# Optimization experiments

Hardware: AMD Instinct MI355X
Metric: run time of the kernel (lower is better)

## Reference

```python
import jax, jax.numpy as jnp
import numpy as np
import math

NUM_HEADS = 16
ROPE_BASE = 10000.0


def _rotate_half(x):
    d = x.shape[-1] // 2
    return jnp.concatenate([-x[..., d:], x[..., :d]], axis=-1)


def setup_inputs() -> dict:
    key = jax.random.key(0)
    ks = jax.random.split(key, 6)
    B, S, H = 2, 2048, 2048
    x = jax.random.normal(ks[0], (B, S, H), dtype=jnp.float32)
    # xavier_uniform for square [H,H]: limit = sqrt(6/(H+H))
    lim = math.sqrt(6.0 / (H + H))
    Wq = jax.random.uniform(ks[1], (H, H), minval=-lim, maxval=lim, dtype=jnp.float32)
    Wk = jax.random.uniform(ks[2], (H, H), minval=-lim, maxval=lim, dtype=jnp.float32)
    Wv = jax.random.uniform(ks[3], (H, H), minval=-lim, maxval=lim, dtype=jnp.float32)
    Wo = jax.random.uniform(ks[4], (H, H), minval=-lim, maxval=lim, dtype=jnp.float32)
    # bias_matrix initialized as tril(randn*0.02), matching _init_weights
    bias_matrix = jnp.tril(jax.random.normal(ks[5], (S, S), dtype=jnp.float32) * 0.02)
    return {"x": x, "Wq": Wq, "Wk": Wk, "Wv": Wv, "Wo": Wo, "bias_matrix": bias_matrix}


def reference(x, Wq, Wk, Wv, Wo, bias_matrix):
    B, S, hidden = x.shape
    H = NUM_HEADS
    D = hidden // H

    # projections (torch Linear: y = x @ W.T)
    def proj(W):
        return jnp.einsum('bsh,eh->bse', x, W).reshape(B, S, H, D).transpose(0, 2, 1, 3)

    q, k, v = proj(Wq), proj(Wk), proj(Wv)  # [B,H,S,D]

    # rotary embeddings
    inv_freq = 1.0 / (ROPE_BASE ** (jnp.arange(0, D, 2, dtype=jnp.float32) / D))
    t = jnp.arange(S, dtype=jnp.float32)
    freqs = t[:, None] * inv_freq[None, :]          # [S, D/2]
    emb = jnp.concatenate([freqs, freqs], axis=-1)  # [S, D]
    cos = jnp.cos(emb)[None, None]                  # [1,1,S,D]
    sin = jnp.sin(emb)[None, None]

    q = q * cos + _rotate_half(q) * sin
    k = k * cos + _rotate_half(k) * sin

    # contextual bias: bias_matrix[:S,:S], broadcast over batch & heads
    bias = bias_matrix[:S, :S][None, None]          # [1,1,S,S]
    bmean = jnp.mean(bias, axis=-1, keepdims=True) * 0.1  # [1,1,S,1]
    q = q + bmean
    k = k + bmean

    scores = jnp.einsum('bhqd,bhkd->bhqk', q, k) / math.sqrt(D)
    scores = scores + bias

    causal = jnp.triu(jnp.ones((S, S), dtype=bool), k=1)
    scores = jnp.where(causal[None, None], -jnp.inf, scores)

    attn_weights = jax.nn.softmax(scores, axis=-1)  # [B,H,S,S]
    attn_out = jnp.einsum('bhqk,bhkd->bhqd', attn_weights, v)
    attn_out = attn_out.transpose(0, 2, 1, 3).reshape(B, S, hidden)
    output = jnp.einsum('bsh,eh->bse', attn_out, Wo)
    return output, attn_weights
```

## Files before the change

kernel.cpp:

```cpp
#include <hip/hip_runtime.h>
#include <hip/hip_bf16.h>

typedef __bf16 bf16_t;
typedef __bf16 bf16x8 __attribute__((ext_vector_type(8)));
typedef float f32x4 __attribute__((ext_vector_type(4)));

#define SEQ 2048
#define HID 2048
#define NH 16
#define DH 128
#define BATCH 2

typedef __attribute__((address_space(1))) const unsigned int g_u32;
typedef __attribute__((address_space(3))) unsigned int l_u32;
#define GLOAD_LDS16(g, l) __builtin_amdgcn_global_load_lds((g_u32*)(g), (l_u32*)(l), 16, 0, 0)

__device__ __forceinline__ unsigned short f2bf(float f) {
  return __builtin_bit_cast(unsigned short, (__bf16)f);
}

__global__ void k_cast_bf16(const float4* __restrict__ in, ushort4* __restrict__ out, int n4) {
  int i = blockIdx.x * 256 + threadIdx.x;
  if (i >= n4) return;
  float4 v = in[i];
  ushort4 o;
  o.x = f2bf(v.x); o.y = f2bf(v.y); o.z = f2bf(v.z); o.w = f2bf(v.w);
  out[i] = o;
}

__global__ void k_bmean(const float* __restrict__ bias, float* __restrict__ bm) {
  int s = blockIdx.x;
  int t = threadIdx.x;
  const float4* row = (const float4*)(bias + (size_t)s * SEQ);
  float acc = 0.f;
  for (int c = t; c < SEQ / 4; c += 256) { float4 v = row[c]; acc += (v.x + v.y) + (v.z + v.w); }
  for (int off = 1; off < 64; off <<= 1) acc += __shfl_xor(acc, off);
  __shared__ float red[4];
  if ((t & 63) == 0) red[t >> 6] = acc;
  __syncthreads();
  if (t == 0) bm[s] = (red[0] + red[1] + red[2] + red[3]) * (0.1f / SEQ);
}

template <int EPI>
__global__ __launch_bounds__(256, 2) void k_gemm_bt(const bf16_t* __restrict__ A,
                                                    const bf16_t* __restrict__ B,
                                                    void* __restrict__ C,
                                                    int M, int N, int K) {
  __shared__ ushort As[128 * 64];
  __shared__ ushort Bs[128 * 64];
  const int tid = threadIdx.x;
  const int lane = tid & 63, wave = tid >> 6;
  const int m16 = lane & 15, quad = lane >> 4;
  const int wm = (wave >> 1) * 64, wn = (wave & 1) * 64;
  const int bm0 = blockIdx.y * 128, bn0 = blockIdx.x * 128;

  f32x4 acc[4][4];
  for (int i = 0; i < 4; ++i)
    for (int j = 0; j < 4; ++j) acc[i][j] = (f32x4){0.f, 0.f, 0.f, 0.f};

  const int NT = K / 64;
  for (int kt = 0; kt < NT; ++kt) {
    __syncthreads();
    size_t k0 = (size_t)kt * 64;
    for (int it = 0; it < 4; ++it) {
      int g = it * 256 + tid;
      int r = g >> 3;
      int c8 = (g & 7) ^ (r & 7);
      int base = (it * 256 + wave * 64) * 8;
      GLOAD_LDS16(A + (size_t)(bm0 + r) * K + k0 + c8 * 8, &As[base]);
      GLOAD_LDS16(B + (size_t)(bn0 + r) * K + k0 + c8 * 8, &Bs[base]);
    }
    __syncthreads();
    for (int ks = 0; ks < 2; ++ks) {
      bf16x8 af[4], bfr[4];
      for (int i = 0; i < 4; ++i) {
        int row = wm + i * 16 + m16;
        af[i] = *(const bf16x8*)&As[row * 64 + (((ks * 4 + quad) ^ (row & 7)) * 8)];
      }
      for (int j = 0; j < 4; ++j) {
        int row = wn + j * 16 + m16;
        bfr[j] = *(const bf16x8*)&Bs[row * 64 + (((ks * 4 + quad) ^ (row & 7)) * 8)];
      }
      for (int i = 0; i < 4; ++i)
        for (int j = 0; j < 4; ++j)
          acc[i][j] = __builtin_amdgcn_mfma_f32_16x16x32_bf16(af[i], bfr[j], acc[i][j], 0, 0, 0);
    }
  }
  for (int i = 0; i < 4; ++i)
    for (int j = 0; j < 4; ++j)
      for (int r = 0; r < 4; ++r) {
        int row = bm0 + wm + i * 16 + quad * 4 + r;
        int col = bn0 + wn + j * 16 + m16;
        float v = acc[i][j][r];
        if (EPI == 0) ((float*)C)[(size_t)row * N + col] = v;
        else          ((bf16_t*)C)[(size_t)row * N + col] = (bf16_t)v;
      }
}

__global__ void k_vtrans(const bf16_t* __restrict__ Vr, bf16_t* __restrict__ Vt) {
  __shared__ ushort T[64 * 72];
  const int tid = threadIdx.x;
  const int s0 = blockIdx.x * 64, c0 = blockIdx.y * 64, b = blockIdx.z;
  const int h = c0 >> 7, d0 = c0 & (DH - 1);
  int r = tid >> 2, cc = (tid & 3) * 16;
  const bf16_t* src = Vr + ((size_t)(b * SEQ + s0 + r)) * HID + c0 + cc;
  *(uint4*)&T[r * 72 + cc] = *(const uint4*)src;
  *(uint4*)&T[r * 72 + cc + 8] = *(const uint4*)(src + 8);
  __syncthreads();
  int dr = tid >> 2, sc0 = (tid & 3) * 16;
  ushort tmp[16];
  for (int e = 0; e < 16; ++e) tmp[e] = T[(sc0 + e) * 72 + dr];
  bf16_t* dst = Vt + ((size_t)(b * NH + h) * DH + d0 + dr) * SEQ + s0 + sc0;
  *(uint4*)dst = *(uint4*)&tmp[0];
  *(uint4*)(dst + 8) = *(uint4*)&tmp[8];
}

__global__ void k_rope(const float* __restrict__ Qf, const float* __restrict__ Kf,
                       const float* __restrict__ bm,
                       bf16_t* __restrict__ Qb, bf16_t* __restrict__ Kb) {
  int idx = blockIdx.x * 256 + threadIdx.x;
  int row = idx >> 10, p = idx & 1023;
  int h = p >> 6, i = p & 63;
  int s = row & (SEQ - 1);
  float invf = powf(10000.f, -(float)i * (1.f / 64.f));
  float ang = (float)s * invf;
  float sn, cs;
  sincosf(ang, &sn, &cs);
  float b = bm[s];
  size_t o1 = (size_t)row * HID + h * DH + i;
  size_t o2 = o1 + 64;
  float q1 = Qf[o1], q2 = Qf[o2];
  Qb[o1] = (bf16_t)(q1 * cs - q2 * sn + b);
  Qb[o2] = (bf16_t)(q2 * cs + q1 * sn + b);
  float k1 = Kf[o1], k2 = Kf[o2];
  Kb[o1] = (bf16_t)(k1 * cs - k2 * sn + b);
  Kb[o2] = (bf16_t)(k2 * cs + k1 * sn + b);
}

__global__ __launch_bounds__(256, 3) void k_attn(const bf16_t* __restrict__ Qb,
                                                 const bf16_t* __restrict__ Kb,
                                                 const bf16_t* __restrict__ Vt,
                                                 const float* __restrict__ bias,
                                                 float* __restrict__ P,
                                                 bf16_t* __restrict__ AO) {
  __shared__ ushort Qs[64 * 128];
  __shared__ ushort Ks[64 * 128];
  __shared__ ushort Ps[64 * 72];
  __shared__ ushort Bs[64 * 68];

  const int tid = threadIdx.x;
  const int lane = tid & 63, wave = tid >> 6;
  const int m16 = lane & 15, quad = lane >> 4;
  const int qb = (int)gridDim.x - 1 - (int)blockIdx.x;
  const int h = blockIdx.y, b = blockIdx.z;
  const int q0 = qb * 64;
  const int wq = wave * 16;
  const float scale = 0.08838834764831845f;

  const bf16_t* Qg = Qb + ((size_t)(b * SEQ + q0)) * HID + (size_t)h * DH;
  for (int it = 0; it < 4; ++it) {
    int g = it * 256 + tid;
    int r = g >> 4;
    int c16 = (g & 15) ^ (r & 15);
    GLOAD_LDS16(Qg + (size_t)r * HID + c16 * 8, &Qs[(it * 256 + wave * 64) * 8]);
  }

  const bf16_t* Kbase = Kb + ((size_t)b * SEQ) * HID + (size_t)h * DH;
  const float* bg = bias + (size_t)q0 * SEQ;

  float m_ln[4], l_ln[4];
  for (int r = 0; r < 4; ++r) { m_ln[r] = -1e30f; l_ln[r] = 0.f; }

  const int bR = tid >> 4, bC = (tid & 15) * 4;
  float4 bpre[4];
  for (int it = 0; it < 4; ++it)
    bpre[it] = *(const float4*)(bg + (size_t)(bR + it * 16) * SEQ + bC);

  for (int kt = 0; kt <= qb; ++kt) {
    __syncthreads();
    const bf16_t* Kg = Kbase + (size_t)(kt * 64) * HID;
    for (int it = 0; it < 4; ++it) {
      int g = it * 256 + tid;
      int r = g >> 4;
      int c16 = (g & 15) ^ (r & 15);
      GLOAD_LDS16(Kg + (size_t)r * HID + c16 * 8, &Ks[(it * 256 + wave * 64) * 8]);
    }
    for (int it = 0; it < 4; ++it) {
      ushort4 o;
      o.x = f2bf(bpre[it].x); o.y = f2bf(bpre[it].y); o.z = f2bf(bpre[it].z); o.w = f2bf(bpre[it].w);
      *(ushort4*)&Bs[(bR + it * 16) * 68 + bC] = o;
    }
    __syncthreads();
    if (kt < qb)
      for (int it = 0; it < 4; ++it)
        bpre[it] = *(const float4*)(bg + (size_t)(bR + it * 16) * SEQ + (kt + 1) * 64 + bC);

    f32x4 sc[4];
    for (int j = 0; j < 4; ++j) sc[j] = (f32x4){0.f, 0.f, 0.f, 0.f};
    for (int ks = 0; ks < 4; ++ks) {
      int qrow = wq + m16;
      bf16x8 af = *(const bf16x8*)&Qs[qrow * 128 + (((ks * 4 + quad) ^ (qrow & 15)) * 8)];
      for (int j = 0; j < 4; ++j) {
        int krow = j * 16 + m16;
        bf16x8 bfr = *(const bf16x8*)&Ks[krow * 128 + (((ks * 4 + quad) ^ (krow & 15)) * 8)];
        sc[j] = __builtin_amdgcn_mfma_f32_16x16x32_bf16(af, bfr, sc[j], 0, 0, 0);
      }
    }
    for (int r = 0; r < 4; ++r) {
      int rl = wq + quad * 4 + r, qi = q0 + rl;
      float v[4], mx = m_ln[r];
      for (int j = 0; j < 4; ++j) {
        int ki = kt * 64 + j * 16 + m16;
        float bv = (float)(*(const bf16_t*)&Bs[rl * 68 + j * 16 + m16]);
        float xv = sc[j][r] * scale + bv;
        v[j] = (ki > qi) ? -1e30f : xv;
        mx = fmaxf(mx, v[j]);
      }
      float corr = __expf(m_ln[r] - mx);
      float s = __expf(v[0] - mx) + __expf(v[1] - mx) + __expf(v[2] - mx) + __expf(v[3] - mx);
      l_ln[r] = l_ln[r] * corr + s;
      m_ln[r] = mx;
    }
  }
  float mrow[4], linv[4];
  for (int r = 0; r < 4; ++r) {
    float m = m_ln[r], l = l_ln[r];
    for (int off = 1; off < 16; off <<= 1) {
      float mo = __shfl_xor(m, off), lo = __shfl_xor(l, off);
      float mn = fmaxf(m, mo);
      l = l * __expf(m - mn) + lo * __expf(mo - mn);
      m = mn;
    }
    mrow[r] = m; linv[r] = 1.f / l;
  }

  f32x4 oacc[8];
  for (int d = 0; d < 8; ++d) oacc[d] = (f32x4){0.f, 0.f, 0.f, 0.f};
  float* Pg = P + (((size_t)(b * NH + h)) * SEQ + q0) * SEQ;
  const bf16_t* Vbase = Vt + ((size_t)(b * NH + h)) * DH * SEQ;

  for (int it = 0; it < 4; ++it)
    bpre[it] = *(const float4*)(bg + (size_t)(bR + it * 16) * SEQ + bC);

  for (int kt = 0; kt <= qb; ++kt) {
    __syncthreads();
    const bf16_t* Kg = Kbase + (size_t)(kt * 64) * HID;
    for (int it = 0; it < 4; ++it) {
      int g = it * 256 + tid;
      int r = g >> 4;
      int c16 = (g & 15) ^ (r & 15);
      GLOAD_LDS16(Kg + (size_t)r * HID + c16 * 8, &Ks[(it * 256 + wave * 64) * 8]);
    }
    for (int it = 0; it < 4; ++it) {
      ushort4 o;
      o.x = f2bf(bpre[it].x); o.y = f2bf(bpre[it].y); o.z = f2bf(bpre[it].z); o.w = f2bf(bpre[it].w);
      *(ushort4*)&Bs[(bR + it * 16) * 68 + bC] = o;
    }
    __syncthreads();
    if (kt < qb)
      for (int it = 0; it < 4; ++it)
        bpre[it] = *(const float4*)(bg + (size_t)(bR + it * 16) * SEQ + (kt + 1) * 64 + bC);

    f32x4 sc[4];
    for (int j = 0; j < 4; ++j) sc[j] = (f32x4){0.f, 0.f, 0.f, 0.f};
    for (int ks = 0; ks < 4; ++ks) {
      int qrow = wq + m16;
      bf16x8 af = *(const bf16x8*)&Qs[qrow * 128 + (((ks * 4 + quad) ^ (qrow & 15)) * 8)];
      for (int j = 0; j < 4; ++j) {
        int krow = j * 16 + m16;
        bf16x8 bfr = *(const bf16x8*)&Ks[krow * 128 + (((ks * 4 + quad) ^ (krow & 15)) * 8)];
        sc[j] = __builtin_amdgcn_mfma_f32_16x16x32_bf16(af, bfr, sc[j], 0, 0, 0);
      }
    }

    bf16x8 vf0[8];
    for (int dt = 0; dt < 8; ++dt)
      vf0[dt] = *(const bf16x8*)(Vbase + (size_t)(dt * 16 + m16) * SEQ + kt * 64 + quad * 8);

    for (int r = 0; r < 4; ++r) {
      int rl = wq + quad * 4 + r, qi = q0 + rl;
      for (int j = 0; j < 4; ++j) {
        int ki = kt * 64 + j * 16 + m16;
        float bv = (float)(*(const bf16_t*)&Bs[rl * 68 + j * 16 + m16]);
        float xv = sc[j][r] * scale + bv;
        float p = (ki > qi) ? 0.f : __expf(xv - mrow[r]) * linv[r];
        Pg[(size_t)rl * SEQ + ki] = p;
        Ps[rl * 72 + j * 16 + m16] = f2bf(p);
      }
    }

    bf16x8 vf1[8];
    for (int dt = 0; dt < 8; ++dt)
      vf1[dt] = *(const bf16x8*)(Vbase + (size_t)(dt * 16 + m16) * SEQ + kt * 64 + 32 + quad * 8);

    {
      bf16x8 pf = *(const bf16x8*)&Ps[(wq + m16) * 72 + quad * 8];
      for (int dt = 0; dt < 8; ++dt)
        oacc[dt] = __builtin_amdgcn_mfma_f32_16x16x32_bf16(pf, vf0[dt], oacc[dt], 0, 0, 0);
      pf = *(const bf16x8*)&Ps[(wq + m16) * 72 + 32 + quad * 8];
      for (int dt = 0; dt < 8; ++dt)
        oacc[dt] = __builtin_amdgcn_mfma_f32_16x16x32_bf16(pf, vf1[dt], oacc[dt], 0, 0, 0);
    }
  }

  bf16_t* AOg = AO + ((size_t)(b * SEQ + q0)) * HID + (size_t)h * DH;
  for (int r = 0; r < 4; ++r) {
    int rl = wq + quad * 4 + r;
    for (int dt = 0; dt < 8; ++dt)
      AOg[(size_t)rl * HID + dt * 16 + m16] = (bf16_t)oacc[dt][r];
  }

  int kz0 = (qb + 1) * 64;
  for (int r = 0; r < 64; ++r) {
    float4* dst = (float4*)(Pg + (size_t)r * SEQ);
    for (int c = kz0 / 4 + tid; c < SEQ / 4; c += 256) dst[c] = make_float4(0.f, 0.f, 0.f, 0.f);
  }
}

extern "C" void kernel_launch(void* const* d_in, const int* in_sizes, int n_in,
                              void* d_out, int out_size, void* d_ws, size_t ws_size,
                              hipStream_t stream) {
  const float* x = (const float*)d_in[0];
  const float* Wq = (const float*)d_in[1];
  const float* Wk = (const float*)d_in[2];
  const float* Wv = (const float*)d_in[3];
  const float* Wo = (const float*)d_in[4];
  const float* bias = (const float*)d_in[5];

  float* out = (float*)d_out;
  float* P = out + (size_t)BATCH * SEQ * HID;
  float* Qf = P;
  float* Kf = P + (size_t)BATCH * SEQ * HID;
  bf16_t* Vr = (bf16_t*)(P + 2 * (size_t)BATCH * SEQ * HID);

  char* w = (char*)d_ws;
  bf16_t* xb = (bf16_t*)w;  w += (size_t)BATCH * SEQ * HID * 2;
  bf16_t* Wqb = (bf16_t*)w; w += (size_t)HID * HID * 2;
  bf16_t* Wkb = (bf16_t*)w; w += (size_t)HID * HID * 2;
  bf16_t* Wvb = (bf16_t*)w; w += (size_t)HID * HID * 2;
  bf16_t* Wob = (bf16_t*)w; w += (size_t)HID * HID * 2;
  bf16_t* Qb = (bf16_t*)w;  w += (size_t)BATCH * SEQ * HID * 2;
  bf16_t* Kb = (bf16_t*)w;  w += (size_t)BATCH * SEQ * HID * 2;
  bf16_t* Vt = (bf16_t*)w;  w += (size_t)BATCH * SEQ * HID * 2;
  bf16_t* AO = (bf16_t*)w;  w += (size_t)BATCH * SEQ * HID * 2;
  float* bm = (float*)w;    w += (size_t)SEQ * 4;

  const int n4x = BATCH * SEQ * HID / 4;
  const int n4w = HID * HID / 4;
  k_cast_bf16<<<(n4x + 255) / 256, 256, 0, stream>>>((const float4*)x, (ushort4*)xb, n4x);
  k_cast_bf16<<<(n4w + 255) / 256, 256, 0, stream>>>((const float4*)Wq, (ushort4*)Wqb, n4w);
  k_cast_bf16<<<(n4w + 255) / 256, 256, 0, stream>>>((const float4*)Wk, (ushort4*)Wkb, n4w);
  k_cast_bf16<<<(n4w + 255) / 256, 256, 0, stream>>>((const float4*)Wv, (ushort4*)Wvb, n4w);
  k_cast_bf16<<<(n4w + 255) / 256, 256, 0, stream>>>((const float4*)Wo, (ushort4*)Wob, n4w);
  k_bmean<<<SEQ, 256, 0, stream>>>(bias, bm);

  dim3 gg(HID / 128, BATCH * SEQ / 128);
  k_gemm_bt<0><<<gg, 256, 0, stream>>>(xb, Wqb, Qf, BATCH * SEQ, HID, HID);
  k_gemm_bt<0><<<gg, 256, 0, stream>>>(xb, Wkb, Kf, BATCH * SEQ, HID, HID);
  k_gemm_bt<1><<<gg, 256, 0, stream>>>(xb, Wvb, Vr, BATCH * SEQ, HID, HID);

  k_vtrans<<<dim3(SEQ / 64, HID / 64, BATCH), 256, 0, stream>>>(Vr, Vt);
  k_rope<<<(BATCH * SEQ * HID / 2) / 256, 256, 0, stream>>>(Qf, Kf, bm, Qb, Kb);

  k_attn<<<dim3(SEQ / 64, NH, BATCH), 256, 0, stream>>>(Qb, Kb, Vt, bias, P, AO);

  k_gemm_bt<0><<<gg, 256, 0, stream>>>(AO, Wob, out, BATCH * SEQ, HID, HID);
}
```

Baseline: 1.231 ms.

## Load Q, K and bias directly into registers, drop LDS staging and barriers

Removes the shared-memory staging of Q, K and the bias tile, along with the two __syncthreads per key tile. Each wave now loads its Q fragments once into registers and reads K fragments and bias values straight from global memory per tile. The probability matrix stores and the zero-fill of the masked region now use nontemporal stores, and many loops gain unroll pragmas. This cuts LDS traffic and synchronisation, at the cost of redundant K loads across the four waves (now served by cache) and less coalesced bias reads in float instead of bf16.

```diff
diff --git a/kernel.cpp b/kernel.cpp
--- a/kernel.cpp
+++ b/kernel.cpp
@@ -143,10 +143,7 @@
                                                  const float* __restrict__ bias,
                                                  float* __restrict__ P,
                                                  bf16_t* __restrict__ AO) {
-  __shared__ ushort Qs[64 * 128];
-  __shared__ ushort Ks[64 * 128];
   __shared__ ushort Ps[64 * 72];
-  __shared__ ushort Bs[64 * 68];
 
   const int tid = threadIdx.x;
   const int lane = tid & 63, wave = tid >> 6;
@@ -157,62 +154,49 @@
   const int wq = wave * 16;
   const float scale = 0.08838834764831845f;
 
-  const bf16_t* Qg = Qb + ((size_t)(b * SEQ + q0)) * HID + (size_t)h * DH;
-  for (int it = 0; it < 4; ++it) {
-    int g = it * 256 + tid;
-    int r = g >> 4;
-    int c16 = (g & 15) ^ (r & 15);
-    GLOAD_LDS16(Qg + (size_t)r * HID + c16 * 8, &Qs[(it * 256 + wave * 64) * 8]);
-  }
-
-  const bf16_t* Kbase = Kb + ((size_t)b * SEQ) * HID + (size_t)h * DH;
-  const float* bg = bias + (size_t)q0 * SEQ;
+  const bf16_t* Qg = Qb + ((size_t)(b * SEQ + q0 + wq + m16)) * HID + (size_t)h * DH;
+  bf16x8 qf[4];
+#pragma unroll
+  for (int ks = 0; ks < 4; ++ks) qf[ks] = *(const bf16x8*)(Qg + ks * 32 + quad * 8);
+
+  const bf16_t* Kbase = Kb + ((size_t)b * SEQ) * HID + (size_t)h * DH + quad * 8;
+  const float* bl = bias + (size_t)(q0 + wq + quad * 4) * SEQ + m16;
 
   float m_ln[4], l_ln[4];
+#pragma unroll
   for (int r = 0; r < 4; ++r) { m_ln[r] = -1e30f; l_ln[r] = 0.f; }
 
-  const int bR = tid >> 4, bC = (tid & 15) * 4;
-  float4 bpre[4];
-  for (int it = 0; it < 4; ++it)
-    bpre[it] = *(const float4*)(bg + (size_t)(bR + it * 16) * SEQ + bC);
-
   for (int kt = 0; kt <= qb; ++kt) {
-    __syncthreads();
-    const bf16_t* Kg = Kbase + (size_t)(kt * 64) * HID;
-    for (int it = 0; it < 4; ++it) {
-      int g = it * 256 + tid;
-      int r = g >> 4;
-      int c16 = (g & 15) ^ (r & 15);
-      GLOAD_LDS16(Kg + (size_t)r * HID + c16 * 8, &Ks[(it * 256 + wave * 64) * 8]);
-    }
-    for (int it = 0; it < 4; ++it) {
-      ushort4 o;
-      o.x = f2bf(bpre[it].x); o.y = f2bf(bpre[it].y); o.z = f2bf(bpre[it].z); o.w = f2bf(bpre[it].w);
-      *(ushort4*)&Bs[(bR + it * 16) * 68 + bC] = o;
-    }
-    __syncthreads();
-    if (kt < qb)
-      for (int it = 0; it < 4; ++it)
-        bpre[it] = *(const float4*)(bg + (size_t)(bR + it * 16) * SEQ + (kt + 1) * 64 + bC);
+    const bf16_t* Kg = Kbase + (size_t)(kt * 64 + m16) * HID;
+    float bv[4][4];
+#pragma unroll
+    for (int r = 0; r < 4; ++r)
+#pragma unroll
+      for (int j = 0; j < 4; ++j) bv[r][j] = bl[(size_t)r * SEQ + kt * 64 + j * 16];
 
     f32x4 sc[4];
+#pragma unroll
     for (int j = 0; j < 4; ++j) sc[j] = (f32x4){0.f, 0.f, 0.f, 0.f};
-    for (int ks = 0; ks < 4; ++ks) {
-      int qrow = wq + m16;
-      bf16x8 af = *(const bf16x8*)&Qs[qrow * 128 + (((ks * 4 + quad) ^ (qrow & 15)) * 8)];
-      for (int j = 0; j < 4; ++j) {
-        int krow = j * 16 + m16;
-        bf16x8 bfr = *(const bf16x8*)&Ks[krow * 128 + (((ks * 4 + quad) ^ (krow & 15)) * 8)];
-        sc[j] = __builtin_amdgcn_mfma_f32_16x16x32_bf16(af, bfr, sc[j], 0, 0, 0);
-      }
-    }
+#pragma unroll
+    for (int j = 0; j < 4; ++j) {
+      const bf16_t* kr = Kg + (size_t)(j * 16) * HID;
+      bf16x8 k0 = *(const bf16x8*)(kr);
+      bf16x8 k1 = *(const bf16x8*)(kr + 32);
+      bf16x8 k2 = *(const bf16x8*)(kr + 64);
+      bf16x8 k3 = *(const bf16x8*)(kr + 96);
+      sc[j] = __builtin_amdgcn_mfma_f32_16x16x32_bf16(qf[0], k0, sc[j], 0, 0, 0);
+      sc[j] = __builtin_amdgcn_mfma_f32_16x16x32_bf16(qf[1], k1, sc[j], 0, 0, 0);
+      sc[j] = __builtin_amdgcn_mfma_f32_16x16x32_bf16(qf[2], k2, sc[j], 0, 0, 0);
+      sc[j] = __builtin_amdgcn_mfma_f32_16x16x32_bf16(qf[3], k3, sc[j], 0, 0, 0);
+    }
+#pragma unroll
     for (int r = 0; r < 4; ++r) {
-      int rl = wq + quad * 4 + r, qi = q0 + rl;
+      int qi = q0 + wq + quad * 4 + r;
       float v[4], mx = m_ln[r];
+#pragma unroll
       for (int j = 0; j < 4; ++j) {
         int ki = kt * 64 + j * 16 + m16;
-        float bv = (float)(*(const bf16_t*)&Bs[rl * 68 + j * 16 + m16]);
-        float xv = sc[j][r] * scale + bv;
+        float xv = sc[j][r] * scale + bv[r][j];
         v[j] = (ki > qi) ? -1e30f : xv;
         mx = fmaxf(mx, v[j]);
       }
@@ -223,6 +207,7 @@
     }
   }
   float mrow[4], linv[4];
+#pragma unroll
   for (int r = 0; r < 4; ++r) {
     float m = m_ln[r], l = l_ln[r];
     for (int off = 1; off < 16; off <<= 1) {
@@ -235,85 +220,85 @@
   }
 
   f32x4 oacc[8];
+#pragma unroll
   for (int d = 0; d < 8; ++d) oacc[d] = (f32x4){0.f, 0.f, 0.f, 0.f};
   float* Pg = P + (((size_t)(b * NH + h)) * SEQ + q0) * SEQ;
   const bf16_t* Vbase = Vt + ((size_t)(b * NH + h)) * DH * SEQ;
 
-  for (int it = 0; it < 4; ++it)
-    bpre[it] = *(const float4*)(bg + (size_t)(bR + it * 16) * SEQ + bC);
-
   for (int kt = 0; kt <= qb; ++kt) {
-    __syncthreads();
-    const bf16_t* Kg = Kbase + (size_t)(kt * 64) * HID;
-    for (int it = 0; it < 4; ++it) {
-      int g = it * 256 + tid;
-      int r = g >> 4;
-      int c16 = (g & 15) ^ (r & 15);
-      GLOAD_LDS16(Kg + (size_t)r * HID + c16 * 8, &Ks[(it * 256 + wave * 64) * 8]);
-    }
-    for (int it = 0; it < 4; ++it) {
-      ushort4 o;
-      o.x = f2bf(bpre[it].x); o.y = f2bf(bpre[it].y); o.z = f2bf(bpre[it].z); o.w = f2bf(bpre[it].w);
-      *(ushort4*)&Bs[(bR + it * 16) * 68 + bC] = o;
-    }
-    __syncthreads();
-    if (kt < qb)
-      for (int it = 0; it < 4; ++it)
-        bpre[it] = *(const float4*)(bg + (size_t)(bR + it * 16) * SEQ + (kt + 1) * 64 + bC);
+    const bf16_t* Kg = Kbase + (size_t)(kt * 64 + m16) * HID;
+    float bv[4][4];
+#pragma unroll
+    for (int r = 0; r < 4; ++r)
+#pragma unroll
+      for (int j = 0; j < 4; ++j) bv[r][j] = bl[(size_t)r * SEQ + kt * 64 + j * 16];
 
     f32x4 sc[4];
+#pragma unroll
     for (int j = 0; j < 4; ++j) sc[j] = (f32x4){0.f, 0.f, 0.f, 0.f};
-    for (int ks = 0; ks < 4; ++ks) {
-      int qrow = wq + m16;
-      bf16x8 af = *(const bf16x8*)&Qs[qrow * 128 + (((ks * 4 + quad) ^ (qrow & 15)) * 8)];
-      for (int j = 0; j < 4; ++j) {
-        int krow = j * 16 + m16;
-        bf16x8 bfr = *(const bf16x8*)&Ks[krow * 128 + (((ks * 4 + quad) ^ (krow & 15)) * 8)];
-        sc[j] = __builtin_amdgcn_mfma_f32_16x16x32_bf16(af, bfr, sc[j], 0, 0, 0);
-      }
+#pragma unroll
+    for (int j = 0; j < 4; ++j) {
+      const bf16_t* kr = Kg + (size_t)(j * 16) * HID;
+      bf16x8 k0 = *(const bf16x8*)(kr);
+      bf16x8 k1 = *(const bf16x8*)(kr + 32);
+      bf16x8 k2 = *(const bf16x8*)(kr + 64);
+      bf16x8 k3 = *(const bf16x8*)(kr + 96);
+      sc[j] = __builtin_amdgcn_mfma_f32_16x16x32_bf16(qf[0], k0, sc[j], 0, 0, 0);
+      sc[j] = __builtin_amdgcn_mfma_f32_16x16x32_bf16(qf[1], k1, sc[j], 0, 0, 0);
+      sc[j] = __builtin_amdgcn_mfma_f32_16x16x32_bf16(qf[2], k2, sc[j], 0, 0, 0);
+      sc[j] = __builtin_amdgcn_mfma_f32_16x16x32_bf16(qf[3], k3, sc[j], 0, 0, 0);
     }
 
     bf16x8 vf0[8];
+#pragma unroll
     for (int dt = 0; dt < 8; ++dt)
       vf0[dt] = *(const bf16x8*)(Vbase + (size_t)(dt * 16 + m16) * SEQ + kt * 64 + quad * 8);
 
+#pragma unroll
     for (int r = 0; r < 4; ++r) {
       int rl = wq + quad * 4 + r, qi = q0 + rl;
+#pragma unroll
       for (int j = 0; j < 4; ++j) {
         int ki = kt * 64 + j * 16 + m16;
-        float bv = (float)(*(const bf16_t*)&Bs[rl * 68 + j * 16 + m16]);
-        float xv = sc[j][r] * scale + bv;
+        float xv = sc[j][r] * scale + bv[r][j];
         float p = (ki > qi) ? 0.f : __expf(xv - mrow[r]) * linv[r];
-        Pg[(size_t)rl * SEQ + ki] = p;
+        __builtin_nontemporal_store(p, Pg + (size_t)rl * SEQ + ki);
         Ps[rl * 72 + j * 16 + m16] = f2bf(p);
       }
     }
 
     bf16x8 vf1[8];
+#pragma unroll
     for (int dt = 0; dt < 8; ++dt)
       vf1[dt] = *(const bf16x8*)(Vbase + (size_t)(dt * 16 + m16) * SEQ + kt * 64 + 32 + quad * 8);
 
     {
       bf16x8 pf = *(const bf16x8*)&Ps[(wq + m16) * 72 + quad * 8];
+#pragma unroll
       for (int dt = 0; dt < 8; ++dt)
         oacc[dt] = __builtin_amdgcn_mfma_f32_16x16x32_bf16(pf, vf0[dt], oacc[dt], 0, 0, 0);
       pf = *(const bf16x8*)&Ps[(wq + m16) * 72 + 32 + quad * 8];
+#pragma unroll
       for (int dt = 0; dt < 8; ++dt)
         oacc[dt] = __builtin_amdgcn_mfma_f32_16x16x32_bf16(pf, vf1[dt], oacc[dt], 0, 0, 0);
     }
   }
 
   bf16_t* AOg = AO + ((size_t)(b * SEQ + q0)) * HID + (size_t)h * DH;
+#pragma unroll
   for (int r = 0; r < 4; ++r) {
     int rl = wq + quad * 4 + r;
+#pragma unroll
     for (int dt = 0; dt < 8; ++dt)
       AOg[(size_t)rl * HID + dt * 16 + m16] = (bf16_t)oacc[dt][r];
   }
 
   int kz0 = (qb + 1) * 64;
+  f32x4 z4 = (f32x4){0.f, 0.f, 0.f, 0.f};
   for (int r = 0; r < 64; ++r) {
-    float4* dst = (float4*)(Pg + (size_t)r * SEQ);
-    for (int c = kz0 / 4 + tid; c < SEQ / 4; c += 256) dst[c] = make_float4(0.f, 0.f, 0.f, 0.f);
+    f32x4* dst = (f32x4*)(Pg + (size_t)r * SEQ);
+    for (int c = kz0 / 4 + tid; c < SEQ / 4; c += 256)
+      __builtin_nontemporal_store(z4, dst + c);
   }
 }
 
```

Result: slower. 1.451 ms (+17.9%).

## Double-buffer K and bias tiles, precast bias to bf16, pair causal query tiles

Applied to the files above, without the earlier changes.

The bias matrix is now cast to bf16 once, into the reused x workspace, and staged into LDS with direct global-to-LDS loads. K and bias tiles are double-buffered so the next tile's loads overlap the current tile's MFMA work. Each block now handles two query tiles (qt and 31-qt) to balance causal work, using a grid half the size. The costs are more LDS per block and launch_bounds lowered to 2 blocks per CU, which may reduce occupancy, plus one extra cast kernel.

```diff
diff --git a/kernel.cpp b/kernel.cpp
--- a/kernel.cpp
+++ b/kernel.cpp
@@ -137,183 +137,201 @@
   Kb[o2] = (bf16_t)(k2 * cs + k1 * sn + b);
 }
 
-__global__ __launch_bounds__(256, 3) void k_attn(const bf16_t* __restrict__ Qb,
+__global__ __launch_bounds__(256, 2) void k_attn(const bf16_t* __restrict__ Qb,
                                                  const bf16_t* __restrict__ Kb,
                                                  const bf16_t* __restrict__ Vt,
-                                                 const float* __restrict__ bias,
+                                                 const bf16_t* __restrict__ Bb,
                                                  float* __restrict__ P,
                                                  bf16_t* __restrict__ AO) {
   __shared__ ushort Qs[64 * 128];
-  __shared__ ushort Ks[64 * 128];
+  __shared__ ushort Ks[2][64 * 128];
+  __shared__ ushort Bs[2][64 * 64];
   __shared__ ushort Ps[64 * 72];
-  __shared__ ushort Bs[64 * 68];
 
   const int tid = threadIdx.x;
   const int lane = tid & 63, wave = tid >> 6;
   const int m16 = lane & 15, quad = lane >> 4;
-  const int qb = (int)gridDim.x - 1 - (int)blockIdx.x;
   const int h = blockIdx.y, b = blockIdx.z;
-  const int q0 = qb * 64;
   const int wq = wave * 16;
   const float scale = 0.08838834764831845f;
 
-  const bf16_t* Qg = Qb + ((size_t)(b * SEQ + q0)) * HID + (size_t)h * DH;
-  for (int it = 0; it < 4; ++it) {
-    int g = it * 256 + tid;
-    int r = g >> 4;
-    int c16 = (g & 15) ^ (r & 15);
-    GLOAD_LDS16(Qg + (size_t)r * HID + c16 * 8, &Qs[(it * 256 + wave * 64) * 8]);
-  }
-
   const bf16_t* Kbase = Kb + ((size_t)b * SEQ) * HID + (size_t)h * DH;
-  const float* bg = bias + (size_t)q0 * SEQ;
-
-  float m_ln[4], l_ln[4];
-  for (int r = 0; r < 4; ++r) { m_ln[r] = -1e30f; l_ln[r] = 0.f; }
-
-  const int bR = tid >> 4, bC = (tid & 15) * 4;
-  float4 bpre[4];
-  for (int it = 0; it < 4; ++it)
-    bpre[it] = *(const float4*)(bg + (size_t)(bR + it * 16) * SEQ + bC);
-
-  for (int kt = 0; kt <= qb; ++kt) {
-    __syncthreads();
+  const bf16_t* Vbase = Vt + ((size_t)(b * NH + h)) * DH * SEQ;
+
+  auto stageK = [&](int kt, int buf) {
     const bf16_t* Kg = Kbase + (size_t)(kt * 64) * HID;
+#pragma unroll
     for (int it = 0; it < 4; ++it) {
       int g = it * 256 + tid;
       int r = g >> 4;
       int c16 = (g & 15) ^ (r & 15);
-      GLOAD_LDS16(Kg + (size_t)r * HID + c16 * 8, &Ks[(it * 256 + wave * 64) * 8]);
-    }
-    for (int it = 0; it < 4; ++it) {
-      ushort4 o;
-      o.x = f2bf(bpre[it].x); o.y = f2bf(bpre[it].y); o.z = f2bf(bpre[it].z); o.w = f2bf(bpre[it].w);
-      *(ushort4*)&Bs[(bR + it * 16) * 68 + bC] = o;
-    }
+      GLOAD_LDS16(Kg + (size_t)r * HID + c16 * 8, &Ks[buf][(it * 256 + wave * 64) * 8]);
+    }
+  };
+
+  for (int half = 0; half < 2; ++half) {
+    const int qt = half ? (int)blockIdx.x : 31 - (int)blockIdx.x;
+    const int q0 = qt * 64;
+    const bf16_t* Bgq = Bb + (size_t)q0 * SEQ;
+
+    auto stageB = [&](int kt, int buf) {
+      const bf16_t* Bg = Bgq + kt * 64;
+#pragma unroll
+      for (int it = 0; it < 2; ++it) {
+        int g = it * 256 + tid;
+        int r = g >> 3;
+        int c8 = (g & 7) ^ (r & 7);
+        GLOAD_LDS16(Bg + (size_t)r * SEQ + c8 * 8, &Bs[buf][(it * 256 + wave * 64) * 8]);
+      }
+    };
+
     __syncthreads();
-    if (kt < qb)
-      for (int it = 0; it < 4; ++it)
-        bpre[it] = *(const float4*)(bg + (size_t)(bR + it * 16) * SEQ + (kt + 1) * 64 + bC);
-
-    f32x4 sc[4];
-    for (int j = 0; j < 4; ++j) sc[j] = (f32x4){0.f, 0.f, 0.f, 0.f};
-    for (int ks = 0; ks < 4; ++ks) {
-      int qrow = wq + m16;
-      bf16x8 af = *(const bf16x8*)&Qs[qrow * 128 + (((ks * 4 + quad) ^ (qrow & 15)) * 8)];
-      for (int j = 0; j < 4; ++j) {
-        int krow = j * 16 + m16;
-        bf16x8 bfr = *(const bf16x8*)&Ks[krow * 128 + (((ks * 4 + quad) ^ (krow & 15)) * 8)];
-        sc[j] = __builtin_amdgcn_mfma_f32_16x16x32_bf16(af, bfr, sc[j], 0, 0, 0);
-      }
-    }
-    for (int r = 0; r < 4; ++r) {
-      int rl = wq + quad * 4 + r, qi = q0 + rl;
-      float v[4], mx = m_ln[r];
-      for (int j = 0; j < 4; ++j) {
-        int ki = kt * 64 + j * 16 + m16;
-        float bv = (float)(*(const bf16_t*)&Bs[rl * 68 + j * 16 + m16]);
-        float xv = sc[j][r] * scale + bv;
-        v[j] = (ki > qi) ? -1e30f : xv;
-        mx = fmaxf(mx, v[j]);
-      }
-      float corr = __expf(m_ln[r] - mx);
-      float s = __expf(v[0] - mx) + __expf(v[1] - mx) + __expf(v[2] - mx) + __expf(v[3] - mx);
-      l_ln[r] = l_ln[r] * corr + s;
-      m_ln[r] = mx;
-    }
-  }
-  float mrow[4], linv[4];
-  for (int r = 0; r < 4; ++r) {
-    float m = m_ln[r], l = l_ln[r];
-    for (int off = 1; off < 16; off <<= 1) {
-      float mo = __shfl_xor(m, off), lo = __shfl_xor(l, off);
-      float mn = fmaxf(m, mo);
-      l = l * __expf(m - mn) + lo * __expf(mo - mn);
-      m = mn;
-    }
-    mrow[r] = m; linv[r] = 1.f / l;
-  }
-
-  f32x4 oacc[8];
-  for (int d = 0; d < 8; ++d) oacc[d] = (f32x4){0.f, 0.f, 0.f, 0.f};
-  float* Pg = P + (((size_t)(b * NH + h)) * SEQ + q0) * SEQ;
-  const bf16_t* Vbase = Vt + ((size_t)(b * NH + h)) * DH * SEQ;
-
-  for (int it = 0; it < 4; ++it)
-    bpre[it] = *(const float4*)(bg + (size_t)(bR + it * 16) * SEQ + bC);
-
-  for (int kt = 0; kt <= qb; ++kt) {
-    __syncthreads();
-    const bf16_t* Kg = Kbase + (size_t)(kt * 64) * HID;
+    const bf16_t* Qg = Qb + ((size_t)(b * SEQ + q0)) * HID + (size_t)h * DH;
+#pragma unroll
     for (int it = 0; it < 4; ++it) {
       int g = it * 256 + tid;
       int r = g >> 4;
       int c16 = (g & 15) ^ (r & 15);
-      GLOAD_LDS16(Kg + (size_t)r * HID + c16 * 8, &Ks[(it * 256 + wave * 64) * 8]);
-    }
-    for (int it = 0; it < 4; ++it) {
-      ushort4 o;
-      o.x = f2bf(bpre[it].x); o.y = f2bf(bpre[it].y); o.z = f2bf(bpre[it].z); o.w = f2bf(bpre[it].w);
-      *(ushort4*)&Bs[(bR + it * 16) * 68 + bC] = o;
-    }
+      GLOAD_LDS16(Qg + (size_t)r * HID + c16 * 8, &Qs[(it * 256 + wave * 64) * 8]);
+    }
+    stageK(0, 0);
+    stageB(0, 0);
+
+    float m_ln[4], l_ln[4];
+#pragma unroll
+    for (int r = 0; r < 4; ++r) { m_ln[r] = -1e30f; l_ln[r] = 0.f; }
+
+    for (int kt = 0; kt <= qt; ++kt) {
+      const int cur = kt & 1;
+      __syncthreads();
+      if (kt < qt) { stageK(kt + 1, cur ^ 1); stageB(kt + 1, cur ^ 1); }
+
+      f32x4 sc[4];
+#pragma unroll
+      for (int j = 0; j < 4; ++j) sc[j] = (f32x4){0.f, 0.f, 0.f, 0.f};
+#pragma unroll
+      for (int ks = 0; ks < 4; ++ks) {
+        int qrow = wq + m16;
+        bf16x8 af = *(const bf16x8*)&Qs[qrow * 128 + (((ks * 4 + quad) ^ (qrow & 15)) * 8)];
+#pragma unroll
+        for (int j = 0; j < 4; ++j) {
+          int krow = j * 16 + m16;
+          bf16x8 bfr = *(const bf16x8*)&Ks[cur][krow * 128 + (((ks * 4 + quad) ^ (krow & 15)) * 8)];
+          sc[j] = __builtin_amdgcn_mfma_f32_16x16x32_bf16(af, bfr, sc[j], 0, 0, 0);
+        }
+      }
+#pragma unroll
+      for (int r = 0; r < 4; ++r) {
+        int rl = wq + quad * 4 + r, qi = q0 + rl;
+        float v[4], mx = m_ln[r];
+#pragma unroll
+        for (int j = 0; j < 4; ++j) {
+          int c = j * 16 + m16;
+          int ki = kt * 64 + c;
+          float bv = (float)(*(const bf16_t*)&Bs[cur][rl * 64 + (((c >> 3) ^ (rl & 7)) << 3) + (c & 7)]);
+          float xv = sc[j][r] * scale + bv;
+          v[j] = (ki > qi) ? -1e30f : xv;
+          mx = fmaxf(mx, v[j]);
+        }
+        float corr = __expf(m_ln[r] - mx);
+        float s = __expf(v[0] - mx) + __expf(v[1] - mx) + __expf(v[2] - mx) + __expf(v[3] - mx);
+        l_ln[r] = l_ln[r] * corr + s;
+        m_ln[r] = mx;
+      }
+    }
+    float mrow[4], linv[4];
+#pragma unroll
+    for (int r = 0; r < 4; ++r) {
+      float m = m_ln[r], l = l_ln[r];
+      for (int off = 1; off < 16; off <<= 1) {
+        float mo = __shfl_xor(m, off), lo = __shfl_xor(l, off);
+        float mn = fmaxf(m, mo);
+        l = l * __expf(m - mn) + lo * __expf(mo - mn);
+        m = mn;
+      }
+      mrow[r] = m; linv[r] = 1.f / l;
+    }
+
     __syncthreads();
-    if (kt < qb)
-      for (int it = 0; it < 4; ++it)
-        bpre[it] = *(const float4*)(bg + (size_t)(bR + it * 16) * SEQ + (kt + 1) * 64 + bC);
-
-    f32x4 sc[4];
-    for (int j = 0; j < 4; ++j) sc[j] = (f32x4){0.f, 0.f, 0.f, 0.f};
-    for (int ks = 0; ks < 4; ++ks) {
-      int qrow = wq + m16;
-      bf16x8 af = *(const bf16x8*)&Qs[qrow * 128 + (((ks * 4 + quad) ^ (qrow & 15)) * 8)];
-      for (int j = 0; j < 4; ++j) {
-        int krow = j * 16 + m16;
-        bf16x8 bfr = *(const bf16x8*)&Ks[krow * 128 + (((ks * 4 + quad) ^ (krow & 15)) * 8)];
-        sc[j] = __builtin_amdgcn_mfma_f32_16x16x32_bf16(af, bfr, sc[j], 0, 0, 0);
-      }
-    }
-
-    bf16x8 vf0[8];
-    for (int dt = 0; dt < 8; ++dt)
-      vf0[dt] = *(const bf16x8*)(Vbase + (size_t)(dt * 16 + m16) * SEQ + kt * 64 + quad * 8);
-
+    stageK(0, 0);
+    stageB(0, 0);
+
+    f32x4 oacc[8];
+#pragma unroll
+    for (int d = 0; d < 8; ++d) oacc[d] = (f32x4){0.f, 0.f, 0.f, 0.f};
+    float* Pg = P + (((size_t)(b * NH + h)) * SEQ + q0) * SEQ;
+
+    for (int kt = 0; kt <= qt; ++kt) {
+      const int cur = kt & 1;
+      __syncthreads();
+      if (kt < qt) { stageK(kt + 1, cur ^ 1); stageB(kt + 1, cur ^ 1); }
+
+      f32x4 sc[4];
+#pragma unroll
+      for (int j = 0; j < 4; ++j) sc[j] = (f32x4){0.f, 0.f, 0.f, 0.f};
+#pragma unroll
+      for (int ks = 0; ks < 4; ++ks) {
+        int qrow = wq + m16;
+        bf16x8 af = *(const bf16x8*)&Qs[qrow * 128 + (((ks * 4 + quad) ^ (qrow & 15)) * 8)];
+#pragma unroll
+        for (int j = 0; j < 4; ++j) {
+          int krow = j * 16 + m16;
+          bf16x8 bfr = *(const bf16x8*)&Ks[cur][krow * 128 + (((ks * 4 + quad) ^ (krow & 15)) * 8)];
+          sc[j] = __builtin_amdgcn_mfma_f32_16x16x32_bf16(af, bfr, sc[j], 0, 0, 0);
+        }
+      }
+
+      bf16x8 vf0[8];
+#pragma unroll
+      for (int dt = 0; dt < 8; ++dt)
+        vf0[dt] = *(const bf16x8*)(Vbase + (size_t)(dt * 16 + m16) * SEQ + kt * 64 + quad * 8);
+
+#pragma unroll
+      for (int r = 0; r < 4; ++r) {
+        int rl = wq + quad * 4 + r, qi = q0 + rl;
+#pragma unroll
+        for (int j = 0; j < 4; ++j) {
+          int c = j * 16 + m16;
+          int ki = kt * 64 + c;
+          float bv = (float)(*(const bf16_t*)&Bs[cur][rl * 64 + (((c >> 3) ^ (rl & 7)) << 3) + (c & 7)]);
+          float xv = sc[j][r] * scale + bv;
+          float p = (ki > qi) ? 0.f : __expf(xv - mrow[r]) * linv[r];
+          Pg[(size_t)rl * SEQ + ki] = p;
+          Ps[rl * 72 + j * 16 + m16] = f2bf(p);
+        }
+      }
+
+      bf16x8 vf1[8];
+#pragma unroll
+      for (int dt = 0; dt < 8; ++dt)
+        vf1[dt] = *(const bf16x8*)(Vbase + (size_t)(dt * 16 + m16) * SEQ + kt * 64 + 32 + quad * 8);
+
+      {
+        bf16x8 pf = *(const bf16x8*)&Ps[(wq + m16) * 72 + quad * 8];
+#pragma unroll
+        for (int dt = 0; dt < 8; ++dt)
+          oacc[dt] = __builtin_amdgcn_mfma_f32_16x16x32_bf16(pf, vf0[dt], oacc[dt], 0, 0, 0);
+        pf = *(const bf16x8*)&Ps[(wq + m16) * 72 + 32 + quad * 8];
+#pragma unroll
+        for (int dt = 0; dt < 8; ++dt)
+          oacc[dt] = __builtin_amdgcn_mfma_f32_16x16x32_bf16(pf, vf1[dt], oacc[dt], 0, 0, 0);
+      }
+    }
+
+    bf16_t* AOg = AO + ((size_t)(b * SEQ + q0)) * HID + (size_t)h * DH;
+#pragma unroll
     for (int r = 0; r < 4; ++r) {
-      int rl = wq + quad * 4 + r, qi = q0 + rl;
-      for (int j = 0; j < 4; ++j) {
-        int ki = kt * 64 + j * 16 + m16;
-        float bv = (float)(*(const bf16_t*)&Bs[rl * 68 + j * 16 + m16]);
-        float xv = sc[j][r] * scale + bv;
-        float p = (ki > qi) ? 0.f : __expf(xv - mrow[r]) * linv[r];
-        Pg[(size_t)rl * SEQ + ki] = p;
-        Ps[rl * 72 + j * 16 + m16] = f2bf(p);
-      }
-    }
-
-    bf16x8 vf1[8];
-    for (int dt = 0; dt < 8; ++dt)
-      vf1[dt] = *(const bf16x8*)(Vbase + (size_t)(dt * 16 + m16) * SEQ + kt * 64 + 32 + quad * 8);
-
-    {
-      bf16x8 pf = *(const bf16x8*)&Ps[(wq + m16) * 72 + quad * 8];
+      int rl = wq + quad * 4 + r;
+#pragma unroll
       for (int dt = 0; dt < 8; ++dt)
-        oacc[dt] = __builtin_amdgcn_mfma_f32_16x16x32_bf16(pf, vf0[dt], oacc[dt], 0, 0, 0);
-      pf = *(const bf16x8*)&Ps[(wq + m16) * 72 + 32 + quad * 8];
-      for (int dt = 0; dt < 8; ++dt)
-        oacc[dt] = __builtin_amdgcn_mfma_f32_16x16x32_bf16(pf, vf1[dt], oacc[dt], 0, 0, 0);
-    }
-  }
-
-  bf16_t* AOg = AO + ((size_t)(b * SEQ + q0)) * HID + (size_t)h * DH;
-  for (int r = 0; r < 4; ++r) {
-    int rl = wq + quad * 4 + r;
-    for (int dt = 0; dt < 8; ++dt)
-      AOg[(size_t)rl * HID + dt * 16 + m16] = (bf16_t)oacc[dt][r];
-  }
-
-  int kz0 = (qb + 1) * 64;
-  for (int r = 0; r < 64; ++r) {
-    float4* dst = (float4*)(Pg + (size_t)r * SEQ);
-    for (int c = kz0 / 4 + tid; c < SEQ / 4; c += 256) dst[c] = make_float4(0.f, 0.f, 0.f, 0.f);
+        AOg[(size_t)rl * HID + dt * 16 + m16] = (bf16_t)oacc[dt][r];
+    }
+
+    int kz0 = (qt + 1) * 64;
+    for (int r = 0; r < 64; ++r) {
+      float4* dst = (float4*)(Pg + (size_t)r * SEQ);
+      for (int c = kz0 / 4 + tid; c < SEQ / 4; c += 256) dst[c] = make_float4(0.f, 0.f, 0.f, 0.f);
+    }
   }
 }
 
@@ -344,9 +362,11 @@
   bf16_t* Vt = (bf16_t*)w;  w += (size_t)BATCH * SEQ * HID * 2;
   bf16_t* AO = (bf16_t*)w;  w += (size_t)BATCH * SEQ * HID * 2;
   float* bm = (float*)w;    w += (size_t)SEQ * 4;
+  bf16_t* Bb = xb;
 
   const int n4x = BATCH * SEQ * HID / 4;
   const int n4w = HID * HID / 4;
+  const int n4b = SEQ * SEQ / 4;
   k_cast_bf16<<<(n4x + 255) / 256, 256, 0, stream>>>((const float4*)x, (ushort4*)xb, n4x);
   k_cast_bf16<<<(n4w + 255) / 256, 256, 0, stream>>>((const float4*)Wq, (ushort4*)Wqb, n4w);
   k_cast_bf16<<<(n4w + 255) / 256, 256, 0, stream>>>((const float4*)Wk, (ushort4*)Wkb, n4w);
@@ -359,10 +379,12 @@
   k_gemm_bt<0><<<gg, 256, 0, stream>>>(xb, Wkb, Kf, BATCH * SEQ, HID, HID);
   k_gemm_bt<1><<<gg, 256, 0, stream>>>(xb, Wvb, Vr, BATCH * SEQ, HID, HID);
 
+  k_cast_bf16<<<(n4b + 255) / 256, 256, 0, stream>>>((const float4*)bias, (ushort4*)Bb, n4b);
+
   k_vtrans<<<dim3(SEQ / 64, HID / 64, BATCH), 256, 0, stream>>>(Vr, Vt);
   k_rope<<<(BATCH * SEQ * HID / 2) / 256, 256, 0, stream>>>(Qf, Kf, bm, Qb, Kb);
 
-  k_attn<<<dim3(SEQ / 64, NH, BATCH), 256, 0, stream>>>(Qb, Kb, Vt, bias, P, AO);
+  k_attn<<<dim3(16, NH, BATCH), 256, 0, stream>>>(Qb, Kb, Vt, Bb, P, AO);
 
   k_gemm_bt<0><<<gg, 256, 0, stream>>>(AO, Wob, out, BATCH * SEQ, HID, HID);
 }
```

New measurement: 1.029 ms. -16.4%, faster.
